# Optimization experiments

Hardware: AMD Instinct MI355X
Metric: run time of the kernel (lower is better)

Reference implementation:

```python
import jax, jax.numpy as jnp
import numpy as np

S, B, D, H = 2048, 2, 1024, 16
DK = D // H


def setup_inputs() -> dict:
    key = jax.random.key(0)
    k1, k2, k3 = jax.random.split(key, 3)
    x = jax.random.normal(k1, (S, B, D), dtype=jnp.float32)
    # xavier-uniform-like scale for weights
    w_qkv = jax.random.normal(k2, (3 * D, D), dtype=jnp.float32) * (1.0 / np.sqrt(D))
    w_out = jax.random.normal(k3, (D, D), dtype=jnp.float32) * (1.0 / np.sqrt(D))
    b_out = jnp.zeros((D,), dtype=jnp.float32)
    return {"x": x, "w_qkv": w_qkv, "w_out": w_out, "b_out": b_out}


def reference(x, w_qkv, w_out, b_out):
    seq_len, batch, d_model = x.shape
    n_heads = H
    d_k = d_model // n_heads
    # qkv projection: [S,B,3D]
    qkv = jnp.einsum('sbd,ed->sbe', x, w_qkv)
    qkv = qkv.reshape(seq_len, batch, 3, n_heads, d_k)
    qkv = jnp.transpose(qkv, (2, 1, 3, 0, 4))  # [3,B,H,S,dk]
    q, k, v = qkv[0], qkv[1], qkv[2]
    scores = jnp.einsum('bhqd,bhkd->bhqk', q, k) / jnp.sqrt(jnp.asarray(d_k, x.dtype))
    causal = jnp.triu(jnp.ones((seq_len, seq_len), dtype=bool), k=1)
    scores = jnp.where(causal[None, None], jnp.asarray(-jnp.inf, scores.dtype), scores)
    weights = jax.nn.softmax(scores, axis=-1)
    out = jnp.einsum('bhqk,bhkd->bhqd', weights, v)  # [B,H,S,dk]
    out = jnp.transpose(out, (2, 0, 1, 3)).reshape(seq_len, batch, d_model)
    return jnp.einsum('sbd,ed->sbe', out, w_out) + b_out
```

## Files before the change

kernel.cpp:

```cpp
#include <hip/hip_runtime.h>
#include <cstdint>

typedef _Float16 f16;
typedef _Float16 f16x4 __attribute__((ext_vector_type(4)));
typedef _Float16 f16x8 __attribute__((ext_vector_type(8)));
typedef float f32x4 __attribute__((ext_vector_type(4)));

#define MFMA16(a, b, c) __builtin_amdgcn_mfma_f32_16x16x32_f16(a, b, c, 0, 0, 0)
#define LOG2E 1.4426950408889634f

__device__ __forceinline__ void gload_lds16(const void* g, void* l) {
    __builtin_amdgcn_global_load_lds((__attribute__((address_space(1))) void*)(g),
                                     (__attribute__((address_space(3))) void*)(l),
                                     16, 0, 0);
}


__global__ void cast_all(const float* __restrict__ x, const float* __restrict__ wqv,
                         const float* __restrict__ wo, f16* __restrict__ out) {
    int i = blockIdx.x * blockDim.x + threadIdx.x;
    const float* src; int li;
    if (i < 1048576)      { src = x;   li = i; }
    else if (i < 1835008) { src = wqv; li = i - 1048576; }
    else                  { src = wo;  li = i - 1835008; }
    float4 v = reinterpret_cast<const float4*>(src)[li];
    f16x4 o = {(f16)v.x, (f16)v.y, (f16)v.z, (f16)v.w};
    reinterpret_cast<f16x4*>(out)[i] = o;
}

__global__ __launch_bounds__(256) void gemm_qkv(
    const f16* __restrict__ A, const f16* __restrict__ B,
    f16* __restrict__ outq, f16* __restrict__ outk, f16* __restrict__ outv)
{
    __shared__ f16 As[128 * 64];
    __shared__ f16 Bs[128 * 64];
    const int tid = threadIdx.x;
    const int lane = tid & 63;
    const int wave = tid >> 6;
    const int wm = wave >> 1, wn = wave & 1;
    const int bm = blockIdx.y * 128, bn = blockIdx.x * 128;
    const int sr = tid >> 3;
    const int scu = (tid & 7) ^ (sr & 7);
    const int fr = lane & 15, fq = lane >> 4;
    const int u0 = (fq ^ (fr & 7)) * 8;
    const int u1 = ((4 + fq) ^ (fr & 7)) * 8;

    f32x4 acc[4][4] = {};

    for (int k0 = 0; k0 < 1024; k0 += 64) {
        __syncthreads();
#pragma unroll
        for (int is = 0; is < 4; ++is) {
            gload_lds16(&A[(bm + sr + is * 32) * 1024 + k0 + scu * 8], &As[is * 2048 + tid * 8]);
            gload_lds16(&B[(bn + sr + is * 32) * 1024 + k0 + scu * 8], &Bs[is * 2048 + tid * 8]);
        }
        __syncthreads();
        f16x8 af0[4], af1[4], bf0[4], bf1[4];
#pragma unroll
        for (int mt = 0; mt < 4; ++mt) {
            int r = wm * 64 + mt * 16 + fr;
            af0[mt] = *(const f16x8*)&As[r * 64 + u0];
            af1[mt] = *(const f16x8*)&As[r * 64 + u1];
        }
#pragma unroll
        for (int nt = 0; nt < 4; ++nt) {
            int r = wn * 64 + nt * 16 + fr;
            bf0[nt] = *(const f16x8*)&Bs[r * 64 + u0];
            bf1[nt] = *(const f16x8*)&Bs[r * 64 + u1];
        }
#pragma unroll
        for (int mt = 0; mt < 4; ++mt)
#pragma unroll
            for (int nt = 0; nt < 4; ++nt) {
                acc[mt][nt] = MFMA16(af0[mt], bf0[nt], acc[mt][nt]);
                acc[mt][nt] = MFMA16(af1[mt], bf1[nt], acc[mt][nt]);
            }
    }

#pragma unroll
    for (int mt = 0; mt < 4; ++mt)
#pragma unroll
        for (int nt = 0; nt < 4; ++nt)
#pragma unroll
            for (int i = 0; i < 4; ++i) {
                int row = bm + wm * 64 + mt * 16 + fq * 4 + i;
                int col = bn + wn * 64 + nt * 16 + fr;
                int s = row >> 1, b = row & 1;
                int which = col >> 10, rem = col & 1023;
                int h = rem >> 6, dk = rem & 63;
                int bh = b * 16 + h;
                float va = acc[mt][nt][i];
                if (which == 0)      outq[(bh * 2048 + s) * 64 + dk] = (f16)(va * 0.125f);
                else if (which == 1) outk[(bh * 2048 + s) * 64 + dk] = (f16)va;
                else                 outv[(bh * 2048 + s) * 64 + dk] = (f16)va;
            }
}

__global__ __launch_bounds__(256) void transpose_v(const f16* __restrict__ v, f16* __restrict__ vt) {
    __shared__ f16 T[64 * 72];
    const int tid = threadIdx.x;
    const int bh = blockIdx.y;
    const int s0 = blockIdx.x * 64;
    const f16* V = v + (bh * 2048 + s0) * 64;
    const int u = tid & 7;
#pragma unroll
    for (int hh = 0; hh < 2; ++hh) {
        int r = (tid >> 3) + hh * 32;
        *(f16x8*)&T[r * 72 + u * 8] = *(const f16x8*)&V[r * 64 + u * 8];
    }
    __syncthreads();
#pragma unroll
    for (int o = 0; o < 2; ++o) {
        int dk = (tid >> 3) + o * 32;
        f16x8 val;
#pragma unroll
        for (int j = 0; j < 8; ++j) val[j] = T[(u * 8 + j) * 72 + dk];
        *(f16x8*)&vt[(bh * 64 + dk) * 2048 + s0 + u * 8] = val;
    }
}

__global__ __launch_bounds__(256) void attn_kernel(
    const f16* __restrict__ qg, const f16* __restrict__ kg,
    const f16* __restrict__ vtg, f16* __restrict__ attn)
{
    __shared__ f16 Ks[2][64 * 64];
    __shared__ f16 Vs[2][64 * 64];
    __shared__ f16 plds[4][16 * 72];
    const int tid = threadIdx.x;
    const int lane = tid & 63;
    const int wave = tid >> 6;
    const int qpair = blockIdx.x;
    const int bh = blockIdx.y;
    const int b = bh >> 4, h = bh & 15;
    const int fr = lane & 15, fq = lane >> 4;

    const int bqA = qpair * 64;
    const int bqB = (31 - qpair) * 64;
    const int nA = qpair + 1;
    const int nB = 32 - qpair;
    const int qrowA = bqA + wave * 16;
    const int qrowB = bqB + wave * 16;

    const f16* Q  = qg  + bh * 2048 * 64;
    const f16* K  = kg  + bh * 2048 * 64;
    const f16* VT = vtg + bh * 64 * 2048;
    f16* P = plds[wave];

    const int sr = tid >> 3;
    const int scu = (tid & 7) ^ (sr & 7);

    f16x8 aqA0 = *(const f16x8*)&Q[(qrowA + fr) * 64 + fq * 8];
    f16x8 aqA1 = *(const f16x8*)&Q[(qrowA + fr) * 64 + 32 + fq * 8];
    f16x8 aqB0 = *(const f16x8*)&Q[(qrowB + fr) * 64 + fq * 8];
    f16x8 aqB1 = *(const f16x8*)&Q[(qrowB + fr) * 64 + 32 + fq * 8];

    f32x4 oA[4] = {}, oB[4] = {};
    float lA[4] = {}, lB[4] = {};

    auto stage = [&](int kc, int buf) {
        const int kb = kc * 64;
        gload_lds16(&K[(kb + sr) * 64 + scu * 8],         &Ks[buf][tid * 8]);
        gload_lds16(&K[(kb + sr + 32) * 64 + scu * 8],    &Ks[buf][2048 + tid * 8]);
        gload_lds16(&VT[sr * 2048 + kb + scu * 8],        &Vs[buf][tid * 8]);
        gload_lds16(&VT[(sr + 32) * 2048 + kb + scu * 8], &Vs[buf][2048 + tid * 8]);
    };

    auto compute = [&](const f16x8& aq0, const f16x8& aq1, int qrow0, int kb,
                       const f16* Ksb, const f16* Vsb, f32x4* oacc, float* li, bool domask) {
        f32x4 sc[4] = {};
#pragma unroll
        for (int ct = 0; ct < 4; ++ct) {
            int r = ct * 16 + fr;
            f16x8 b0 = *(const f16x8*)&Ksb[r * 64 + ((fq ^ (r & 7)) * 8)];
            f16x8 b1 = *(const f16x8*)&Ksb[r * 64 + (((4 + fq) ^ (r & 7)) * 8)];
            sc[ct] = MFMA16(aq0, b0, sc[ct]);
            sc[ct] = MFMA16(aq1, b1, sc[ct]);
        }
        if (domask) {
#pragma unroll
            for (int ct = 0; ct < 4; ++ct) {
                int kcol = kb + ct * 16 + fr;
#pragma unroll
                for (int i = 0; i < 4; ++i)
                    if (kcol > qrow0 + fq * 4 + i) sc[ct][i] = -1e30f;
            }
        }
#pragma unroll
        for (int i = 0; i < 4; ++i) {
            float p0 = __builtin_amdgcn_exp2f(sc[0][i] * LOG2E);
            float p1 = __builtin_amdgcn_exp2f(sc[1][i] * LOG2E);
            float p2 = __builtin_amdgcn_exp2f(sc[2][i] * LOG2E);
            float p3 = __builtin_amdgcn_exp2f(sc[3][i] * LOG2E);
            li[i] += (p0 + p1) + (p2 + p3);
            P[(fq * 4 + i) * 72 + fr]      = (f16)p0;
            P[(fq * 4 + i) * 72 + 16 + fr] = (f16)p1;
            P[(fq * 4 + i) * 72 + 32 + fr] = (f16)p2;
            P[(fq * 4 + i) * 72 + 48 + fr] = (f16)p3;
        }
        f16x8 ap0 = *(const f16x8*)&P[fr * 72 + fq * 8];
        f16x8 ap1 = *(const f16x8*)&P[fr * 72 + 32 + fq * 8];
#pragma unroll
        for (int nt = 0; nt < 4; ++nt) {
            int dk = nt * 16 + fr;
            f16x8 bv0 = *(const f16x8*)&Vsb[dk * 64 + ((fq ^ (dk & 7)) * 8)];
            f16x8 bv1 = *(const f16x8*)&Vsb[dk * 64 + (((4 + fq) ^ (dk & 7)) * 8)];
            oacc[nt] = MFMA16(ap0, bv0, oacc[nt]);
            oacc[nt] = MFMA16(ap1, bv1, oacc[nt]);
        }
    };

    stage(0, 0);
    for (int kc = 0; kc < nB; ++kc) {
        const int kb = kc * 64;
        const int cur = kc & 1;
        __syncthreads();
        if (kc + 1 < nB) stage(kc + 1, cur ^ 1);
        compute(aqB0, aqB1, qrowB, kb, Ks[cur], Vs[cur], oB, lB, kb + 63 > qrowB);
        if (kc < nA)
            compute(aqA0, aqA1, qrowA, kb, Ks[cur], Vs[cur], oA, lA, kb + 63 > qrowA);
    }

#pragma unroll
    for (int i = 0; i < 4; ++i) {
        float rs = lA[i];
        rs += __shfl_xor(rs, 1);
        rs += __shfl_xor(rs, 2);
        rs += __shfl_xor(rs, 4);
        rs += __shfl_xor(rs, 8);
        float inv = __builtin_amdgcn_rcpf(rs);
        int srow = qrowA + fq * 4 + i;
#pragma unroll
        for (int nt = 0; nt < 4; ++nt)
            attn[(srow * 2 + b) * 1024 + h * 64 + nt * 16 + fr] = (f16)(oA[nt][i] * inv);
    }
#pragma unroll
    for (int i = 0; i < 4; ++i) {
        float rs = lB[i];
        rs += __shfl_xor(rs, 1);
        rs += __shfl_xor(rs, 2);
        rs += __shfl_xor(rs, 4);
        rs += __shfl_xor(rs, 8);
        float inv = __builtin_amdgcn_rcpf(rs);
        int srow = qrowB + fq * 4 + i;
#pragma unroll
        for (int nt = 0; nt < 4; ++nt)
            attn[(srow * 2 + b) * 1024 + h * 64 + nt * 16 + fr] = (f16)(oB[nt][i] * inv);
    }
}

__global__ __launch_bounds__(256) void gemm_out(
    const f16* __restrict__ A, const f16* __restrict__ B,
    const float* __restrict__ bias, float* __restrict__ out)
{
    __shared__ f16 As[128 * 64];
    __shared__ f16 Bs[64 * 64];
    const int tid = threadIdx.x;
    const int lane = tid & 63;
    const int wave = tid >> 6;
    const int wm = wave >> 1, wn = wave & 1;
    const int bm = blockIdx.y * 128, bn = blockIdx.x * 64;
    const int sr = tid >> 3;
    const int scu = (tid & 7) ^ (sr & 7);
    const int fr = lane & 15, fq = lane >> 4;
    const int u0 = (fq ^ (fr & 7)) * 8;
    const int u1 = ((4 + fq) ^ (fr & 7)) * 8;

    f32x4 acc[4][2] = {};

    for (int k0 = 0; k0 < 1024; k0 += 64) {
        __syncthreads();
#pragma unroll
        for (int is = 0; is < 4; ++is)
            gload_lds16(&A[(bm + sr + is * 32) * 1024 + k0 + scu * 8], &As[is * 2048 + tid * 8]);
#pragma unroll
        for (int is = 0; is < 2; ++is)
            gload_lds16(&B[(bn + sr + is * 32) * 1024 + k0 + scu * 8], &Bs[is * 2048 + tid * 8]);
        __syncthreads();
        f16x8 af0[4], af1[4], bf0[2], bf1[2];
#pragma unroll
        for (int mt = 0; mt < 4; ++mt) {
            int r = wm * 64 + mt * 16 + fr;
            af0[mt] = *(const f16x8*)&As[r * 64 + u0];
            af1[mt] = *(const f16x8*)&As[r * 64 + u1];
        }
#pragma unroll
        for (int nt = 0; nt < 2; ++nt) {
            int r = wn * 32 + nt * 16 + fr;
            bf0[nt] = *(const f16x8*)&Bs[r * 64 + u0];
            bf1[nt] = *(const f16x8*)&Bs[r * 64 + u1];
        }
#pragma unroll
        for (int mt = 0; mt < 4; ++mt)
#pragma unroll
            for (int nt = 0; nt < 2; ++nt) {
                acc[mt][nt] = MFMA16(af0[mt], bf0[nt], acc[mt][nt]);
                acc[mt][nt] = MFMA16(af1[mt], bf1[nt], acc[mt][nt]);
            }
    }

#pragma unroll
    for (int mt = 0; mt < 4; ++mt)
#pragma unroll
        for (int nt = 0; nt < 2; ++nt)
#pragma unroll
            for (int i = 0; i < 4; ++i) {
                int row = bm + wm * 64 + mt * 16 + fq * 4 + i;
                int col = bn + wn * 32 + nt * 16 + fr;
                out[row * 1024 + col] = acc[mt][nt][i] + bias[col];
            }
}

extern "C" void kernel_launch(void* const* d_in, const int* in_sizes, int n_in,
                              void* d_out, int out_size, void* d_ws, size_t ws_size,
                              hipStream_t stream)
{
    const float* x     = (const float*)d_in[0];
    const float* w_qkv = (const float*)d_in[1];
    const float* w_out = (const float*)d_in[2];
    const float* b_out = (const float*)d_in[3];
    float* out = (float*)d_out;

    char* ws = (char*)d_ws;
    f16* xh  = (f16*)(ws);
    f16* vt  = (f16*)(ws);
    f16* wqh = (f16*)(ws + 8388608);
    f16* woh = (f16*)(ws + 14680064);
    f16* qh  = (f16*)(ws + 16777216);
    f16* kh  = (f16*)(ws + 25165824);
    f16* vh  = (f16*)(ws + 33554432);
    f16* ah  = (f16*)(ws + 41943040);

    cast_all<<<8192, 256, 0, stream>>>(x, w_qkv, w_out, xh);
    gemm_qkv<<<dim3(24, 32), 256, 0, stream>>>(xh, wqh, qh, kh, vh);
    transpose_v<<<dim3(32, 32), 256, 0, stream>>>(vh, vt);
    attn_kernel<<<dim3(16, 32), 256, 0, stream>>>(qh, kh, vt, ah);
    gemm_out<<<dim3(16, 32), 256, 0, stream>>>(ah, woh, b_out, out);
}
```

Before: 188.4 us.

## Rewrite attention with 32x32 MFMA, transposed scores and register-resident P

The attention kernel now uses 32x32x16 MFMAs and computes transposed scores (K times Q), so each lane owns one query row. The P tile is passed to the PV MFMA through packed half-precision registers and a cross-half lane shuffle instead of an LDS round trip. Work per block changes from paired 64-row query tiles to one 128-row tile, with interleaved block ordering for load balance, and each wave skips 32-key subtiles that are fully masked. Launch bounds request 3 blocks per CU. The trade-off is higher register pressure and less even per-block work than the old pairing scheme.

```diff
diff --git a/kernel.cpp b/kernel.cpp
--- a/kernel.cpp
+++ b/kernel.cpp
@@ -2,17 +2,26 @@
 #include <cstdint>
 
 typedef _Float16 f16;
+typedef _Float16 f16x2 __attribute__((ext_vector_type(2)));
 typedef _Float16 f16x4 __attribute__((ext_vector_type(4)));
 typedef _Float16 f16x8 __attribute__((ext_vector_type(8)));
 typedef float f32x4 __attribute__((ext_vector_type(4)));
+typedef float f32x16 __attribute__((ext_vector_type(16)));
+typedef int i32x4 __attribute__((ext_vector_type(4)));
 
 #define MFMA16(a, b, c) __builtin_amdgcn_mfma_f32_16x16x32_f16(a, b, c, 0, 0, 0)
+#define MFMA32(a, b, c) __builtin_amdgcn_mfma_f32_32x32x16_f16(a, b, c, 0, 0, 0)
 #define LOG2E 1.4426950408889634f
 
 __device__ __forceinline__ void gload_lds16(const void* g, void* l) {
     __builtin_amdgcn_global_load_lds((__attribute__((address_space(1))) void*)(g),
                                      (__attribute__((address_space(3))) void*)(l),
                                      16, 0, 0);
+}
+
+__device__ __forceinline__ int pk2(float a, float b) {
+    f16x2 t = {(f16)a, (f16)b};
+    return __builtin_bit_cast(int, t);
 }
 
 
@@ -119,43 +128,38 @@
     }
 }
 
-__global__ __launch_bounds__(256) void attn_kernel(
+__global__ __launch_bounds__(256, 3) void attn_kernel(
     const f16* __restrict__ qg, const f16* __restrict__ kg,
     const f16* __restrict__ vtg, f16* __restrict__ attn)
 {
     __shared__ f16 Ks[2][64 * 64];
     __shared__ f16 Vs[2][64 * 64];
-    __shared__ f16 plds[4][16 * 72];
     const int tid = threadIdx.x;
     const int lane = tid & 63;
     const int wave = tid >> 6;
-    const int qpair = blockIdx.x;
+    const int xx = blockIdx.x;
+    const int qb2 = (xx & 1) ? (xx >> 1) : (15 - (xx >> 1));
     const int bh = blockIdx.y;
     const int b = bh >> 4, h = bh & 15;
-    const int fr = lane & 15, fq = lane >> 4;
-
-    const int bqA = qpair * 64;
-    const int bqB = (31 - qpair) * 64;
-    const int nA = qpair + 1;
-    const int nB = 32 - qpair;
-    const int qrowA = bqA + wave * 16;
-    const int qrowB = bqB + wave * 16;
+    const int col = lane & 31;
+    const int H = lane >> 5;
+    const int qrow0 = qb2 * 128 + wave * 32;
+    const int qmax = qrow0 + 31;
 
     const f16* Q  = qg  + bh * 2048 * 64;
     const f16* K  = kg  + bh * 2048 * 64;
     const f16* VT = vtg + bh * 64 * 2048;
-    f16* P = plds[wave];
 
     const int sr = tid >> 3;
     const int scu = (tid & 7) ^ (sr & 7);
 
-    f16x8 aqA0 = *(const f16x8*)&Q[(qrowA + fr) * 64 + fq * 8];
-    f16x8 aqA1 = *(const f16x8*)&Q[(qrowA + fr) * 64 + 32 + fq * 8];
-    f16x8 aqB0 = *(const f16x8*)&Q[(qrowB + fr) * 64 + fq * 8];
-    f16x8 aqB1 = *(const f16x8*)&Q[(qrowB + fr) * 64 + 32 + fq * 8];
-
-    f32x4 oA[4] = {}, oB[4] = {};
-    float lA[4] = {}, lB[4] = {};
+    f16x8 qf[4];
+#pragma unroll
+    for (int c = 0; c < 4; ++c)
+        qf[c] = *(const f16x8*)&Q[(qrow0 + col) * 64 + c * 16 + H * 8];
+
+    f32x16 oT[2] = {};
+    float li = 0.f;
 
     auto stage = [&](int kc, int buf) {
         const int kb = kc * 64;
@@ -165,87 +169,78 @@
         gload_lds16(&VT[(sr + 32) * 2048 + kb + scu * 8], &Vs[buf][2048 + tid * 8]);
     };
 
-    auto compute = [&](const f16x8& aq0, const f16x8& aq1, int qrow0, int kb,
-                       const f16* Ksb, const f16* Vsb, f32x4* oacc, float* li, bool domask) {
-        f32x4 sc[4] = {};
-#pragma unroll
-        for (int ct = 0; ct < 4; ++ct) {
-            int r = ct * 16 + fr;
-            f16x8 b0 = *(const f16x8*)&Ksb[r * 64 + ((fq ^ (r & 7)) * 8)];
-            f16x8 b1 = *(const f16x8*)&Ksb[r * 64 + (((4 + fq) ^ (r & 7)) * 8)];
-            sc[ct] = MFMA16(aq0, b0, sc[ct]);
-            sc[ct] = MFMA16(aq1, b1, sc[ct]);
-        }
-        if (domask) {
-#pragma unroll
-            for (int ct = 0; ct < 4; ++ct) {
-                int kcol = kb + ct * 16 + fr;
-#pragma unroll
-                for (int i = 0; i < 4; ++i)
-                    if (kcol > qrow0 + fq * 4 + i) sc[ct][i] = -1e30f;
-            }
-        }
-#pragma unroll
-        for (int i = 0; i < 4; ++i) {
-            float p0 = __builtin_amdgcn_exp2f(sc[0][i] * LOG2E);
-            float p1 = __builtin_amdgcn_exp2f(sc[1][i] * LOG2E);
-            float p2 = __builtin_amdgcn_exp2f(sc[2][i] * LOG2E);
-            float p3 = __builtin_amdgcn_exp2f(sc[3][i] * LOG2E);
-            li[i] += (p0 + p1) + (p2 + p3);
-            P[(fq * 4 + i) * 72 + fr]      = (f16)p0;
-            P[(fq * 4 + i) * 72 + 16 + fr] = (f16)p1;
-            P[(fq * 4 + i) * 72 + 32 + fr] = (f16)p2;
-            P[(fq * 4 + i) * 72 + 48 + fr] = (f16)p3;
-        }
-        f16x8 ap0 = *(const f16x8*)&P[fr * 72 + fq * 8];
-        f16x8 ap1 = *(const f16x8*)&P[fr * 72 + 32 + fq * 8];
-#pragma unroll
-        for (int nt = 0; nt < 4; ++nt) {
-            int dk = nt * 16 + fr;
-            f16x8 bv0 = *(const f16x8*)&Vsb[dk * 64 + ((fq ^ (dk & 7)) * 8)];
-            f16x8 bv1 = *(const f16x8*)&Vsb[dk * 64 + (((4 + fq) ^ (dk & 7)) * 8)];
-            oacc[nt] = MFMA16(ap0, bv0, oacc[nt]);
-            oacc[nt] = MFMA16(ap1, bv1, oacc[nt]);
-        }
-    };
-
+    const int nc = 2 * qb2 + 2;
     stage(0, 0);
-    for (int kc = 0; kc < nB; ++kc) {
+    for (int kc = 0; kc < nc; ++kc) {
         const int kb = kc * 64;
         const int cur = kc & 1;
         __syncthreads();
-        if (kc + 1 < nB) stage(kc + 1, cur ^ 1);
-        compute(aqB0, aqB1, qrowB, kb, Ks[cur], Vs[cur], oB, lB, kb + 63 > qrowB);
-        if (kc < nA)
-            compute(aqA0, aqA1, qrowA, kb, Ks[cur], Vs[cur], oA, lA, kb + 63 > qrowA);
-    }
-
-#pragma unroll
-    for (int i = 0; i < 4; ++i) {
-        float rs = lA[i];
-        rs += __shfl_xor(rs, 1);
-        rs += __shfl_xor(rs, 2);
-        rs += __shfl_xor(rs, 4);
-        rs += __shfl_xor(rs, 8);
-        float inv = __builtin_amdgcn_rcpf(rs);
-        int srow = qrowA + fq * 4 + i;
-#pragma unroll
-        for (int nt = 0; nt < 4; ++nt)
-            attn[(srow * 2 + b) * 1024 + h * 64 + nt * 16 + fr] = (f16)(oA[nt][i] * inv);
-    }
-#pragma unroll
-    for (int i = 0; i < 4; ++i) {
-        float rs = lB[i];
-        rs += __shfl_xor(rs, 1);
-        rs += __shfl_xor(rs, 2);
-        rs += __shfl_xor(rs, 4);
-        rs += __shfl_xor(rs, 8);
-        float inv = __builtin_amdgcn_rcpf(rs);
-        int srow = qrowB + fq * 4 + i;
-#pragma unroll
-        for (int nt = 0; nt < 4; ++nt)
-            attn[(srow * 2 + b) * 1024 + h * 64 + nt * 16 + fr] = (f16)(oB[nt][i] * inv);
-    }
+        if (kc + 1 < nc) stage(kc + 1, cur ^ 1);
+        const f16* Kb = Ks[cur];
+        const f16* Vb = Vs[cur];
+
+#pragma unroll
+        for (int kt = 0; kt < 2; ++kt) {
+            const int kt0 = kb + kt * 32;
+            if (kt0 > qmax) continue;
+
+            f32x16 sc = {};
+#pragma unroll
+            for (int c = 0; c < 4; ++c) {
+                int r = kt * 32 + col;
+                f16x8 ak = *(const f16x8*)&Kb[r * 64 + (((c * 2 + H) ^ (r & 7)) * 8)];
+                sc = MFMA32(ak, qf[c], sc);
+            }
+            if (kt0 + 31 > qrow0) {
+                int q = qrow0 + col;
+#pragma unroll
+                for (int r = 0; r < 16; ++r) {
+                    int key = kt0 + (r & 3) + 8 * (r >> 2) + 4 * H;
+                    if (key > q) sc[r] = -1e30f;
+                }
+            }
+#pragma unroll
+            for (int r = 0; r < 16; ++r) {
+                float p = __builtin_amdgcn_exp2f(sc[r] * LOG2E);
+                li += p;
+                sc[r] = p;
+            }
+            int pk[8], xk[8];
+#pragma unroll
+            for (int g = 0; g < 8; ++g) pk[g] = pk2(sc[2 * g], sc[2 * g + 1]);
+#pragma unroll
+            for (int g = 0; g < 8; ++g) xk[g] = __shfl_xor(pk[g], 32);
+#pragma unroll
+            for (int c2 = 0; c2 < 2; ++c2) {
+                i32x4 bi;
+                bi.x = H ? xk[4 * c2 + 2] : pk[4 * c2];
+                bi.y = H ? xk[4 * c2 + 3] : pk[4 * c2 + 1];
+                bi.z = H ? pk[4 * c2 + 2] : xk[4 * c2];
+                bi.w = H ? pk[4 * c2 + 3] : xk[4 * c2 + 1];
+                f16x8 pb = __builtin_bit_cast(f16x8, bi);
+                const int sub = kt * 2 + c2;
+#pragma unroll
+                for (int dt = 0; dt < 2; ++dt) {
+                    int rv = dt * 32 + col;
+                    f16x8 av = *(const f16x8*)&Vb[rv * 64 + (((sub * 2 + H) ^ (rv & 7)) * 8)];
+                    oT[dt] = MFMA32(av, pb, oT[dt]);
+                }
+            }
+        }
+    }
+
+    li += __shfl_xor(li, 32);
+    float inv = __builtin_amdgcn_rcpf(li);
+    const int q = qrow0 + col;
+    f16* dst = &attn[(q * 2 + b) * 1024 + h * 64];
+#pragma unroll
+    for (int dt = 0; dt < 2; ++dt)
+#pragma unroll
+        for (int g = 0; g < 4; ++g) {
+            f16x4 pv = {(f16)(oT[dt][4 * g] * inv),     (f16)(oT[dt][4 * g + 1] * inv),
+                        (f16)(oT[dt][4 * g + 2] * inv), (f16)(oT[dt][4 * g + 3] * inv)};
+            *(f16x4*)&dst[dt * 32 + 8 * g + 4 * H] = pv;
+        }
 }
 
 __global__ __launch_bounds__(256) void gemm_out(
```

After: 195.6 us. +3.9%, slower.

## Fuse V transpose into QKV GEMM epilogue and fold log2e into Q scale

Applied to the files above, without the earlier changes.

Removes the separate transpose_v kernel by writing V directly in transposed layout from the QKV GEMM epilogue, staging through LDS with padded rows. Q/K epilogue now branches per block rather than per element. Q is prescaled by log2(e)/sqrt(dk), so the softmax exp2 no longer multiplies by LOG2E. This saves one launch, an 8MB write and reread of V, and per-element multiplies, at the cost of extra syncs and LDS traffic in the GEMM epilogue.

```diff
diff --git a/kernel.cpp b/kernel.cpp
--- a/kernel.cpp
+++ b/kernel.cpp
@@ -7,7 +7,7 @@
 typedef float f32x4 __attribute__((ext_vector_type(4)));
 
 #define MFMA16(a, b, c) __builtin_amdgcn_mfma_f32_16x16x32_f16(a, b, c, 0, 0, 0)
-#define LOG2E 1.4426950408889634f
+#define QSCALE 0.1803368801111243f
 
 __device__ __forceinline__ void gload_lds16(const void* g, void* l) {
     __builtin_amdgcn_global_load_lds((__attribute__((address_space(1))) void*)(g),
@@ -30,10 +30,11 @@
 
 __global__ __launch_bounds__(256) void gemm_qkv(
     const f16* __restrict__ A, const f16* __restrict__ B,
-    f16* __restrict__ outq, f16* __restrict__ outk, f16* __restrict__ outv)
+    f16* __restrict__ outq, f16* __restrict__ outk, f16* __restrict__ outvt)
 {
-    __shared__ f16 As[128 * 64];
-    __shared__ f16 Bs[128 * 64];
+    __shared__ f16 SM[128 * 64 * 2];
+    f16* As = SM;
+    f16* Bs = SM + 8192;
     const int tid = threadIdx.x;
     const int lane = tid & 63;
     const int wave = tid >> 6;
@@ -77,45 +78,53 @@
             }
     }
 
-#pragma unroll
-    for (int mt = 0; mt < 4; ++mt)
-#pragma unroll
-        for (int nt = 0; nt < 4; ++nt)
-#pragma unroll
-            for (int i = 0; i < 4; ++i) {
-                int row = bm + wm * 64 + mt * 16 + fq * 4 + i;
-                int col = bn + wn * 64 + nt * 16 + fr;
-                int s = row >> 1, b = row & 1;
-                int which = col >> 10, rem = col & 1023;
-                int h = rem >> 6, dk = rem & 63;
-                int bh = b * 16 + h;
-                float va = acc[mt][nt][i];
-                if (which == 0)      outq[(bh * 2048 + s) * 64 + dk] = (f16)(va * 0.125f);
-                else if (which == 1) outk[(bh * 2048 + s) * 64 + dk] = (f16)va;
-                else                 outv[(bh * 2048 + s) * 64 + dk] = (f16)va;
-            }
-}
-
-__global__ __launch_bounds__(256) void transpose_v(const f16* __restrict__ v, f16* __restrict__ vt) {
-    __shared__ f16 T[64 * 72];
-    const int tid = threadIdx.x;
-    const int bh = blockIdx.y;
-    const int s0 = blockIdx.x * 64;
-    const f16* V = v + (bh * 2048 + s0) * 64;
-    const int u = tid & 7;
-#pragma unroll
-    for (int hh = 0; hh < 2; ++hh) {
-        int r = (tid >> 3) + hh * 32;
-        *(f16x8*)&T[r * 72 + u * 8] = *(const f16x8*)&V[r * 64 + u * 8];
-    }
-    __syncthreads();
-#pragma unroll
-    for (int o = 0; o < 2; ++o) {
-        int dk = (tid >> 3) + o * 32;
-        f16x8 val;
-#pragma unroll
-        for (int j = 0; j < 8; ++j) val[j] = T[(u * 8 + j) * 72 + dk];
-        *(f16x8*)&vt[(bh * 64 + dk) * 2048 + s0 + u * 8] = val;
+    const int x = blockIdx.x;
+    if (x < 16) {
+        f16* base = (x < 8) ? outq : outk;
+        const float scale = (x < 8) ? QSCALE : 1.0f;
+        const int coloff = (x < 8) ? bn : (bn - 1024);
+#pragma unroll
+        for (int mt = 0; mt < 4; ++mt)
+#pragma unroll
+            for (int nt = 0; nt < 4; ++nt)
+#pragma unroll
+                for (int i = 0; i < 4; ++i) {
+                    int row = bm + wm * 64 + mt * 16 + fq * 4 + i;
+                    int col = coloff + wn * 64 + nt * 16 + fr;
+                    int s = row >> 1, b = row & 1;
+                    int h = col >> 6, dk = col & 63;
+                    base[((b * 16 + h) * 2048 + s) * 64 + dk] = (f16)(acc[mt][nt][i] * scale);
+                }
+    } else {
+        const int xb = x - 16;
+        const int s0 = bm >> 1;
+        f16* Ts = SM;
+#pragma unroll
+        for (int p = 0; p < 2; ++p) {
+            __syncthreads();
+            if (wn == p) {
+#pragma unroll
+                for (int mt = 0; mt < 4; ++mt)
+#pragma unroll
+                    for (int nt = 0; nt < 4; ++nt)
+#pragma unroll
+                        for (int i = 0; i < 4; ++i) {
+                            int row = wm * 64 + mt * 16 + fq * 4 + i;
+                            int cl = nt * 16 + fr;
+                            Ts[(cl * 2 + (row & 1)) * 76 + (row >> 1)] = (f16)acc[mt][nt][i];
+                        }
+            }
+            __syncthreads();
+            const int h = xb * 2 + p;
+            const int sj = tid & 7;
+#pragma unroll
+            for (int it = 0; it < 4; ++it) {
+                int idx = (tid >> 3) + it * 32;
+                int bsel = idx & 1, dk = idx >> 1;
+                f16x8 v = *(const f16x8*)&Ts[(dk * 2 + bsel) * 76 + sj * 8];
+                *(f16x8*)&outvt[((bsel * 16 + h) * 64 + dk) * 2048 + s0 + sj * 8] = v;
+            }
+        }
     }
 }
 
@@ -187,10 +196,10 @@
         }
 #pragma unroll
         for (int i = 0; i < 4; ++i) {
-            float p0 = __builtin_amdgcn_exp2f(sc[0][i] * LOG2E);
-            float p1 = __builtin_amdgcn_exp2f(sc[1][i] * LOG2E);
-            float p2 = __builtin_amdgcn_exp2f(sc[2][i] * LOG2E);
-            float p3 = __builtin_amdgcn_exp2f(sc[3][i] * LOG2E);
+            float p0 = __builtin_amdgcn_exp2f(sc[0][i]);
+            float p1 = __builtin_amdgcn_exp2f(sc[1][i]);
+            float p2 = __builtin_amdgcn_exp2f(sc[2][i]);
+            float p3 = __builtin_amdgcn_exp2f(sc[3][i]);
             li[i] += (p0 + p1) + (p2 + p3);
             P[(fq * 4 + i) * 72 + fr]      = (f16)p0;
             P[(fq * 4 + i) * 72 + 16 + fr] = (f16)p1;
@@ -322,17 +331,15 @@
 
     char* ws = (char*)d_ws;
     f16* xh  = (f16*)(ws);
-    f16* vt  = (f16*)(ws);
     f16* wqh = (f16*)(ws + 8388608);
     f16* woh = (f16*)(ws + 14680064);
     f16* qh  = (f16*)(ws + 16777216);
     f16* kh  = (f16*)(ws + 25165824);
-    f16* vh  = (f16*)(ws + 33554432);
+    f16* vt  = (f16*)(ws + 33554432);
     f16* ah  = (f16*)(ws + 41943040);
 
     cast_all<<<8192, 256, 0, stream>>>(x, w_qkv, w_out, xh);
-    gemm_qkv<<<dim3(24, 32), 256, 0, stream>>>(xh, wqh, qh, kh, vh);
-    transpose_v<<<dim3(32, 32), 256, 0, stream>>>(vh, vt);
+    gemm_qkv<<<dim3(24, 32), 256, 0, stream>>>(xh, wqh, qh, kh, vt);
     attn_kernel<<<dim3(16, 32), 256, 0, stream>>>(qh, kh, vt, ah);
     gemm_out<<<dim3(16, 32), 256, 0, stream>>>(ah, woh, b_out, out);
 }
```

Result: no change. 185.8 us (-1.4%).
